# Kernel tuning notes

Hardware: AMD Instinct MI355X
Metric: run time of the kernel (lower is better)

Reference implementation:

```python
import jax, jax.numpy as jnp
import numpy as np

N_EMBD = 2048
HEAD_SIZE = 64  # ln1.weight.shape[0] // n_head = 2048 // 32


def setup_inputs() -> dict:
    key = jax.random.key(0)
    ks = jax.random.split(key, 10)
    B, S, D = 4, 2048, N_EMBD
    return {
        'x': jax.random.normal(ks[0], (B, S, D), jnp.float32),
        'state': jax.random.normal(ks[1], (B, 2 + HEAD_SIZE, D), jnp.float32),
        'time_maa_x': jax.random.uniform(ks[2], (D,), jnp.float32),
        'time_maa_w1': jax.random.normal(ks[3], (D, 160), jnp.float32) * 0.02,
        'time_maa_w2': jax.random.normal(ks[4], (5, 32, D), jnp.float32) * 0.02,
        'maa_k': jax.random.uniform(ks[5], (D,), jnp.float32),
        'maa_w': jax.random.uniform(ks[6], (D,), jnp.float32),
        'maa_v': jax.random.uniform(ks[7], (D,), jnp.float32),
        'maa_r': jax.random.uniform(ks[8], (D,), jnp.float32),
        'maa_g': jax.random.uniform(ks[9], (D,), jnp.float32),
        'i': 0,
    }


def reference(x, state, time_maa_x, time_maa_w1, time_maa_w2,
              maa_k, maa_w, maa_v, maa_r, maa_g, i):
    B, S, D = x.shape
    i1 = (2 + HEAD_SIZE) * i + 1  # state row holding last token of this layer
    # token shift: sx[t] = x[t-1] - x[t], with state row for t=0
    sx = jnp.concatenate([(state[:, i1] - x[:, 0])[:, None],
                          x[:, :-1] - x[:, 1:]], axis=1)  # [B,S,D]
    new_state = state.at[:, i1].set(x[:, -1])
    # LoRA-style mixing coefficients
    xxx = jnp.tanh((x + sx * time_maa_x) @ time_maa_w1)       # [B,S,160]
    xxx = xxx.reshape(B, S, 5, 32)
    xxx = jnp.einsum('bsfk,fkd->bsfd', xxx, time_maa_w2)      # [B,S,5,D]
    stacked = jnp.stack([maa_k, maa_w, maa_v, maa_r, maa_g], axis=0)  # [5,D]
    # broadcast combine across the 5 mixing modes (k,w,v,r,g)
    x_kwvrg = x[:, :, None] + sx[:, :, None] * (stacked + xxx)  # [B,S,5,D]
    return x_kwvrg, new_state
```

## Files before the change

kernel.cpp:

```cpp
#include <hip/hip_runtime.h>

#define DDIM 2048
#define SLEN 2048
#define BSZ 4
#define NTOK (BSZ*SLEN)
#define RANK 160
#define SROWS 66
#define OUT_MAIN ((size_t)NTOK*5*DDIM)
#define STATE_N (BSZ*SROWS*DDIM)

typedef __bf16 bf16x8 __attribute__((ext_vector_type(8)));
typedef float  f32x4  __attribute__((ext_vector_type(4)));
typedef unsigned short us8 __attribute__((ext_vector_type(8)));
typedef unsigned short us4 __attribute__((ext_vector_type(4)));

__device__ __forceinline__ unsigned short f2bf(float f) {
    unsigned b = __float_as_uint(f);
    return (unsigned short)((b + 0x7fffu + ((b >> 16) & 1u)) >> 16);
}

__global__ __launch_bounds__(256) void k_prep(
        const float* __restrict__ x,
        const float* __restrict__ state,
        const int* __restrict__ pi,
        const float* __restrict__ w1,
        const float* __restrict__ w2,
        float* __restrict__ out_state,
        unsigned short* __restrict__ w1t,
        unsigned short* __restrict__ w2t) {
    __shared__ float t[32 * 33];
    int bid = blockIdx.x, tid = threadIdx.x;
    if (bid < 320) {
        int kt = bid / 5;
        int k0 = kt * 32, n0 = (bid - kt * 5) * 32;
        int rr = tid >> 3, cc = (tid & 7) * 4;
        f32x4 v = *(const f32x4*)(w1 + (size_t)(k0 + rr) * RANK + n0 + cc);
        #pragma unroll
        for (int j = 0; j < 4; j++) t[(cc + j) * 33 + rr] = v[j];
        __syncthreads();
        us4 o;
        #pragma unroll
        for (int j = 0; j < 4; j++) o[j] = f2bf(t[rr * 33 + cc + j]);
        *(us4*)(w1t + (size_t)(n0 + rr) * DDIM + k0 + cc) = o;
    } else if (bid < 640) {
        int b2 = bid - 320;
        int f = b2 >> 6, d0 = (b2 & 63) * 32;
        int rr = tid >> 3, cc = (tid & 7) * 4;
        f32x4 v = *(const f32x4*)(w2 + (size_t)(f * 32 + rr) * DDIM + d0 + cc);
        #pragma unroll
        for (int j = 0; j < 4; j++) t[(cc + j) * 33 + rr] = v[j];
        __syncthreads();
        us4 o;
        #pragma unroll
        for (int j = 0; j < 4; j++) o[j] = f2bf(t[rr * 33 + cc + j]);
        *(us4*)(w2t + ((size_t)(f * DDIM) + d0 + rr) * 32 + cc) = o;
    } else {
        int idx = ((bid - 640) * 256 + tid) * 4;
        int i1 = 66 * pi[0] + 1;
        int b   = idx / (SROWS * DDIM);
        int rem = idx - b * (SROWS * DDIM);
        int row = rem / DDIM;
        int d   = rem - row * DDIM;
        f32x4 v;
        if (row == i1) v = *(const f32x4*)(x + ((size_t)(b * SLEN + SLEN - 1)) * DDIM + d);
        else           v = *(const f32x4*)(state + idx);
        *(f32x4*)(out_state + idx) = v;
    }
}

__global__ __launch_bounds__(640) void k_gemm1f(
        const float* __restrict__ x,
        const float* __restrict__ state,
        const float* __restrict__ tmx,
        const unsigned short* __restrict__ w1t,
        const int* __restrict__ pi,
        unsigned short* __restrict__ xxx) {
    __shared__ unsigned short sxw[16 * 136];
    __shared__ float red[10 * 16 * 17];
    int tid  = threadIdx.x;
    int w    = tid >> 6, lane = tid & 63;
    int q    = lane >> 4, nl = lane & 15;
    int kh   = (w >= 5) ? 1 : 0;
    int nh   = kh ? (w - 5) : w;
    int m0   = blockIdx.x * 16;
    int b    = m0 >> 11;
    int i1   = 66 * pi[0] + 1;

    int srow = tid >> 5;
    int scol = (tid & 31) * 4;
    const float* xrow = nullptr;
    const float* prow = nullptr;
    if (tid < 512) {
        int m = m0 + srow;
        int s = m & (SLEN - 1);
        xrow = x + (size_t)m * DDIM;
        prow = (s == 0) ? (state + (size_t)(b * SROWS + i1) * DDIM)
                        : (x + (size_t)(m - 1) * DDIM);
    }

    f32x4 acc[2];
    acc[0] = (f32x4){0.f, 0.f, 0.f, 0.f};
    acc[1] = (f32x4){0.f, 0.f, 0.f, 0.f};

    for (int i = 0; i < 16; i++) {
        if (tid < 512) {
            int gc = i * 128 + scol;
            f32x4 xa = *(const f32x4*)(xrow + gc);
            f32x4 pa = *(const f32x4*)(prow + gc);
            f32x4 ta = *(const f32x4*)(tmx  + gc);
            us4 o;
            #pragma unroll
            for (int j = 0; j < 4; j++)
                o[j] = f2bf(xa[j] + (pa[j] - xa[j]) * ta[j]);
            *(us4*)(sxw + srow * 136 + scol) = o;
        }
        __syncthreads();
        #pragma unroll
        for (int kk = 0; kk < 64; kk += 32) {
            bf16x8 a = *(const bf16x8*)(sxw + nl * 136 + kh * 64 + kk + q * 8);
            #pragma unroll
            for (int t = 0; t < 2; t++) {
                bf16x8 bb = *(const bf16x8*)(w1t + (size_t)(nh * 32 + t * 16 + nl) * DDIM
                                             + i * 128 + kh * 64 + kk + q * 8);
                acc[t] = __builtin_amdgcn_mfma_f32_16x16x32_bf16(a, bb, acc[t], 0, 0, 0);
            }
        }
        __syncthreads();
    }

    if (kh) {
        #pragma unroll
        for (int t = 0; t < 2; t++)
            #pragma unroll
            for (int r = 0; r < 4; r++)
                red[((nh * 2 + t) * 16 + q * 4 + r) * 17 + nl] = acc[t][r];
    }
    __syncthreads();
    if (!kh) {
        #pragma unroll
        for (int t = 0; t < 2; t++)
            #pragma unroll
            for (int r = 0; r < 4; r++) {
                float v = acc[t][r] + red[((nh * 2 + t) * 16 + q * 4 + r) * 17 + nl];
                xxx[(size_t)(m0 + q * 4 + r) * RANK + nh * 32 + t * 16 + nl]
                    = f2bf(tanhf(v));
            }
    }
}

__global__ __launch_bounds__(256) void k_gemm2_out(
        const unsigned short* __restrict__ xxx,
        const unsigned short* __restrict__ w2t,
        const float* __restrict__ x,
        const float* __restrict__ state,
        const float* __restrict__ mk,
        const float* __restrict__ mw,
        const float* __restrict__ mv,
        const float* __restrict__ mr,
        const float* __restrict__ mg,
        const int* __restrict__ pi,
        float* __restrict__ out) {
    __shared__ float res[5 * 16 * 132];
    int tid = threadIdx.x;
    int w = tid >> 6, lane = tid & 63;
    int q = lane >> 4, nl = lane & 15;
    int tokTile = blockIdx.x >> 4;
    int dTile   = blockIdx.x & 15;
    int m0 = tokTile * 16;
    int d0 = dTile * 128;

    for (int t = w; t < 40; t += 4) {
        int f = t >> 3, dsub = t & 7;
        bf16x8 a = *(const bf16x8*)(xxx + (size_t)(m0 + nl) * RANK + f * 32 + q * 8);
        bf16x8 b = *(const bf16x8*)(w2t + ((size_t)(f * DDIM) + d0 + dsub * 16 + nl) * 32 + q * 8);
        f32x4 acc = (f32x4){0.f, 0.f, 0.f, 0.f};
        acc = __builtin_amdgcn_mfma_f32_16x16x32_bf16(a, b, acc, 0, 0, 0);
        #pragma unroll
        for (int r = 0; r < 4; r++)
            res[(f * 16 + q * 4 + r) * 132 + dsub * 16 + nl] = acc[r];
    }
    __syncthreads();

    int i1 = 66 * pi[0] + 1;
    int b     = m0 >> 11;
    int sbase = m0 & (SLEN - 1);
    #pragma unroll
    for (int half = 0; half < 2; half++) {
        int tt  = half * 256 + tid;
        int tok = tt >> 5;
        int dv  = (tt & 31) * 4;
        int s   = sbase + tok;
        int d   = d0 + dv;
        size_t xoff = ((size_t)(b * SLEN + s)) * DDIM + d;
        f32x4 xv = *(const f32x4*)(x + xoff);
        f32x4 pv;
        if (s == 0) pv = *(const f32x4*)(state + ((size_t)(b * SROWS + i1)) * DDIM + d);
        else        pv = *(const f32x4*)(x + xoff - DDIM);
        size_t obase = ((size_t)((b * SLEN + s) * 5)) * DDIM + d;
        #pragma unroll
        for (int f = 0; f < 5; f++) {
            const float* maa = (f == 0) ? mk : (f == 1) ? mw : (f == 2) ? mv
                             : (f == 3) ? mr : mg;
            f32x4 mvv = *(const f32x4*)(maa + d);
            f32x4 rr  = *(const f32x4*)&res[(f * 16 + tok) * 132 + dv];
            f32x4 o;
            #pragma unroll
            for (int j = 0; j < 4; j++) {
                float xf = xv[j];
                float sx = pv[j] - xf;
                o[j] = xf + sx * (mvv[j] + rr[j]);
            }
            *(f32x4*)(out + obase + (size_t)f * DDIM) = o;
        }
    }
}

extern "C" void kernel_launch(void* const* d_in, const int* in_sizes, int n_in,
                              void* d_out, int out_size, void* d_ws, size_t ws_size,
                              hipStream_t stream) {
    const float* x   = (const float*)d_in[0];
    const float* st  = (const float*)d_in[1];
    const float* tmx = (const float*)d_in[2];
    const float* w1  = (const float*)d_in[3];
    const float* w2  = (const float*)d_in[4];
    const float* mk  = (const float*)d_in[5];
    const float* mw  = (const float*)d_in[6];
    const float* mv  = (const float*)d_in[7];
    const float* mr  = (const float*)d_in[8];
    const float* mg  = (const float*)d_in[9];
    const int* pi    = (const int*)d_in[10];
    float* out = (float*)d_out;

    char* ws = (char*)d_ws;
    unsigned short* xxx = (unsigned short*)(ws);
    unsigned short* w1t = (unsigned short*)(ws + 2621440);
    unsigned short* w2t = (unsigned short*)(ws + 2621440 + 655360);

    k_prep<<<1168, 256, 0, stream>>>(x, st, pi, w1, w2, out + OUT_MAIN, w1t, w2t);
    k_gemm1f<<<512, 640, 0, stream>>>(x, st, tmx, w1t, pi, xxx);
    k_gemm2_out<<<8192, 256, 0, stream>>>(xxx, w2t, x, st, mk, mw, mv, mr, mg, pi, out);
}
```

Measured before the change: 459.6 us.

## Fuse LoRA GEMM1, tanh, GEMM2 and output mixing into one kernel

Merges the first projection GEMM (with tanh) and the second per-mode GEMM plus mixing epilogue into a single kernel per 16-token tile. The bf16 intermediate stays in shared memory instead of making a global round trip, and one launch is removed. Each of 5 waves handles one mixing mode and streams across all 2048 channels with scalar nontemporal stores. This gives far fewer blocks and narrower memory accesses than the previous 8192-block epilogue, which risks underusing bandwidth.

```diff
diff --git a/kernel.cpp b/kernel.cpp
--- a/kernel.cpp
+++ b/kernel.cpp
@@ -68,91 +68,12 @@
     }
 }
 
-__global__ __launch_bounds__(640) void k_gemm1f(
+__global__ __launch_bounds__(320, 4) void k_fused(
         const float* __restrict__ x,
         const float* __restrict__ state,
         const float* __restrict__ tmx,
         const unsigned short* __restrict__ w1t,
-        const int* __restrict__ pi,
-        unsigned short* __restrict__ xxx) {
-    __shared__ unsigned short sxw[16 * 136];
-    __shared__ float red[10 * 16 * 17];
-    int tid  = threadIdx.x;
-    int w    = tid >> 6, lane = tid & 63;
-    int q    = lane >> 4, nl = lane & 15;
-    int kh   = (w >= 5) ? 1 : 0;
-    int nh   = kh ? (w - 5) : w;
-    int m0   = blockIdx.x * 16;
-    int b    = m0 >> 11;
-    int i1   = 66 * pi[0] + 1;
-
-    int srow = tid >> 5;
-    int scol = (tid & 31) * 4;
-    const float* xrow = nullptr;
-    const float* prow = nullptr;
-    if (tid < 512) {
-        int m = m0 + srow;
-        int s = m & (SLEN - 1);
-        xrow = x + (size_t)m * DDIM;
-        prow = (s == 0) ? (state + (size_t)(b * SROWS + i1) * DDIM)
-                        : (x + (size_t)(m - 1) * DDIM);
-    }
-
-    f32x4 acc[2];
-    acc[0] = (f32x4){0.f, 0.f, 0.f, 0.f};
-    acc[1] = (f32x4){0.f, 0.f, 0.f, 0.f};
-
-    for (int i = 0; i < 16; i++) {
-        if (tid < 512) {
-            int gc = i * 128 + scol;
-            f32x4 xa = *(const f32x4*)(xrow + gc);
-            f32x4 pa = *(const f32x4*)(prow + gc);
-            f32x4 ta = *(const f32x4*)(tmx  + gc);
-            us4 o;
-            #pragma unroll
-            for (int j = 0; j < 4; j++)
-                o[j] = f2bf(xa[j] + (pa[j] - xa[j]) * ta[j]);
-            *(us4*)(sxw + srow * 136 + scol) = o;
-        }
-        __syncthreads();
-        #pragma unroll
-        for (int kk = 0; kk < 64; kk += 32) {
-            bf16x8 a = *(const bf16x8*)(sxw + nl * 136 + kh * 64 + kk + q * 8);
-            #pragma unroll
-            for (int t = 0; t < 2; t++) {
-                bf16x8 bb = *(const bf16x8*)(w1t + (size_t)(nh * 32 + t * 16 + nl) * DDIM
-                                             + i * 128 + kh * 64 + kk + q * 8);
-                acc[t] = __builtin_amdgcn_mfma_f32_16x16x32_bf16(a, bb, acc[t], 0, 0, 0);
-            }
-        }
-        __syncthreads();
-    }
-
-    if (kh) {
-        #pragma unroll
-        for (int t = 0; t < 2; t++)
-            #pragma unroll
-            for (int r = 0; r < 4; r++)
-                red[((nh * 2 + t) * 16 + q * 4 + r) * 17 + nl] = acc[t][r];
-    }
-    __syncthreads();
-    if (!kh) {
-        #pragma unroll
-        for (int t = 0; t < 2; t++)
-            #pragma unroll
-            for (int r = 0; r < 4; r++) {
-                float v = acc[t][r] + red[((nh * 2 + t) * 16 + q * 4 + r) * 17 + nl];
-                xxx[(size_t)(m0 + q * 4 + r) * RANK + nh * 32 + t * 16 + nl]
-                    = f2bf(tanhf(v));
-            }
-    }
-}
-
-__global__ __launch_bounds__(256) void k_gemm2_out(
-        const unsigned short* __restrict__ xxx,
         const unsigned short* __restrict__ w2t,
-        const float* __restrict__ x,
-        const float* __restrict__ state,
         const float* __restrict__ mk,
         const float* __restrict__ mw,
         const float* __restrict__ mv,
@@ -160,57 +81,121 @@
         const float* __restrict__ mg,
         const int* __restrict__ pi,
         float* __restrict__ out) {
-    __shared__ float res[5 * 16 * 132];
-    int tid = threadIdx.x;
-    int w = tid >> 6, lane = tid & 63;
-    int q = lane >> 4, nl = lane & 15;
-    int tokTile = blockIdx.x >> 4;
-    int dTile   = blockIdx.x & 15;
-    int m0 = tokTile * 16;
-    int d0 = dTile * 128;
-
-    for (int t = w; t < 40; t += 4) {
-        int f = t >> 3, dsub = t & 7;
-        bf16x8 a = *(const bf16x8*)(xxx + (size_t)(m0 + nl) * RANK + f * 32 + q * 8);
-        bf16x8 b = *(const bf16x8*)(w2t + ((size_t)(f * DDIM) + d0 + dsub * 16 + nl) * 32 + q * 8);
-        f32x4 acc = (f32x4){0.f, 0.f, 0.f, 0.f};
-        acc = __builtin_amdgcn_mfma_f32_16x16x32_bf16(a, b, acc, 0, 0, 0);
-        #pragma unroll
-        for (int r = 0; r < 4; r++)
-            res[(f * 16 + q * 4 + r) * 132 + dsub * 16 + nl] = acc[r];
-    }
-    __syncthreads();
-
-    int i1 = 66 * pi[0] + 1;
-    int b     = m0 >> 11;
-    int sbase = m0 & (SLEN - 1);
-    #pragma unroll
-    for (int half = 0; half < 2; half++) {
-        int tt  = half * 256 + tid;
-        int tok = tt >> 5;
-        int dv  = (tt & 31) * 4;
-        int s   = sbase + tok;
-        int d   = d0 + dv;
-        size_t xoff = ((size_t)(b * SLEN + s)) * DDIM + d;
-        f32x4 xv = *(const f32x4*)(x + xoff);
-        f32x4 pv;
-        if (s == 0) pv = *(const f32x4*)(state + ((size_t)(b * SROWS + i1)) * DDIM + d);
-        else        pv = *(const f32x4*)(x + xoff - DDIM);
-        size_t obase = ((size_t)((b * SLEN + s) * 5)) * DDIM + d;
-        #pragma unroll
-        for (int f = 0; f < 5; f++) {
-            const float* maa = (f == 0) ? mk : (f == 1) ? mw : (f == 2) ? mv
-                             : (f == 3) ? mr : mg;
-            f32x4 mvv = *(const f32x4*)(maa + d);
-            f32x4 rr  = *(const f32x4*)&res[(f * 16 + tok) * 132 + dv];
-            f32x4 o;
+    __shared__ unsigned short sxw[16 * 136];
+    __shared__ unsigned short xxxt[16 * 168];
+
+    int tid  = threadIdx.x;
+    int w    = tid >> 6, lane = tid & 63;
+    int q    = lane >> 4, nl = lane & 15;
+    int m0   = blockIdx.x * 16;
+    int b    = m0 >> 11;
+    int i1   = 66 * pi[0] + 1;
+
+    int srow = tid >> 4;
+    int scol = (tid & 15) * 8;
+    const float* xrow = nullptr;
+    const float* prow = nullptr;
+    if (tid < 256) {
+        int m = m0 + srow;
+        int s = m & (SLEN - 1);
+        xrow = x + (size_t)m * DDIM;
+        prow = (s == 0) ? (state + (size_t)(b * SROWS + i1) * DDIM)
+                        : (x + (size_t)(m - 1) * DDIM);
+    }
+
+    f32x4 acc0 = (f32x4){0.f, 0.f, 0.f, 0.f};
+    f32x4 acc1 = (f32x4){0.f, 0.f, 0.f, 0.f};
+
+    for (int k0 = 0; k0 < DDIM; k0 += 128) {
+        if (tid < 256) {
+            f32x4 xa = *(const f32x4*)(xrow + k0 + scol);
+            f32x4 xb = *(const f32x4*)(xrow + k0 + scol + 4);
+            f32x4 pa = *(const f32x4*)(prow + k0 + scol);
+            f32x4 pb = *(const f32x4*)(prow + k0 + scol + 4);
+            f32x4 ta = *(const f32x4*)(tmx  + k0 + scol);
+            f32x4 tb = *(const f32x4*)(tmx  + k0 + scol + 4);
+            us8 o;
             #pragma unroll
             for (int j = 0; j < 4; j++) {
-                float xf = xv[j];
-                float sx = pv[j] - xf;
-                o[j] = xf + sx * (mvv[j] + rr[j]);
-            }
-            *(f32x4*)(out + obase + (size_t)f * DDIM) = o;
+                o[j]     = f2bf(xa[j] + (pa[j] - xa[j]) * ta[j]);
+                o[j + 4] = f2bf(xb[j] + (pb[j] - xb[j]) * tb[j]);
+            }
+            *(us8*)(sxw + srow * 136 + scol) = o;
+        }
+        __syncthreads();
+        #pragma unroll
+        for (int kk = 0; kk < 128; kk += 32) {
+            bf16x8 a  = *(const bf16x8*)(sxw + nl * 136 + kk + q * 8);
+            bf16x8 b0 = *(const bf16x8*)(w1t + (size_t)(w * 32 + nl) * DDIM + k0 + kk + q * 8);
+            bf16x8 b1 = *(const bf16x8*)(w1t + (size_t)(w * 32 + 16 + nl) * DDIM + k0 + kk + q * 8);
+            acc0 = __builtin_amdgcn_mfma_f32_16x16x32_bf16(a, b0, acc0, 0, 0, 0);
+            acc1 = __builtin_amdgcn_mfma_f32_16x16x32_bf16(a, b1, acc1, 0, 0, 0);
+        }
+        __syncthreads();
+    }
+
+    #pragma unroll
+    for (int r = 0; r < 4; r++) {
+        xxxt[(q * 4 + r) * 168 + w * 32 + nl]      = f2bf(tanhf(acc0[r]));
+        xxxt[(q * 4 + r) * 168 + w * 32 + 16 + nl] = f2bf(tanhf(acc1[r]));
+    }
+    __syncthreads();
+
+    const float* maa = (w == 0) ? mk : (w == 1) ? mw : (w == 2) ? mv
+                     : (w == 3) ? mr : mg;
+    bf16x8 af = *(const bf16x8*)(xxxt + nl * 168 + w * 32 + q * 8);
+
+    const float* xb0; const float* xb1; const float* xb2; const float* xb3;
+    const float* pb0; const float* pb1; const float* pb2; const float* pb3;
+    float* ob0; float* ob1; float* ob2; float* ob3;
+    {
+        const float* strow = state + (size_t)(b * SROWS + i1) * DDIM;
+        int t0 = q * 4;
+        int m_ = m0 + t0;
+        xb0 = x + (size_t)m_ * DDIM;
+        pb0 = ((m_ & (SLEN - 1)) == 0) ? strow : (x + (size_t)(m_ - 1) * DDIM);
+        ob0 = (float*)out + ((size_t)(m_ * 5 + w)) * DDIM;
+        m_ = m0 + t0 + 1;
+        xb1 = x + (size_t)m_ * DDIM;
+        pb1 = x + (size_t)(m_ - 1) * DDIM;
+        ob1 = (float*)out + ((size_t)(m_ * 5 + w)) * DDIM;
+        m_ = m0 + t0 + 2;
+        xb2 = x + (size_t)m_ * DDIM;
+        pb2 = x + (size_t)(m_ - 1) * DDIM;
+        ob2 = (float*)out + ((size_t)(m_ * 5 + w)) * DDIM;
+        m_ = m0 + t0 + 3;
+        xb3 = x + (size_t)m_ * DDIM;
+        pb3 = x + (size_t)(m_ - 1) * DDIM;
+        ob3 = (float*)out + ((size_t)(m_ * 5 + w)) * DDIM;
+    }
+
+    const unsigned short* w2base = w2t + ((size_t)w * DDIM) * 32;
+
+    for (int dT = 0; dT < 16; dT++) {
+        int d0 = dT * 128;
+        #pragma unroll 2
+        for (int dsub = 0; dsub < 8; dsub++) {
+            int d = d0 + dsub * 16 + nl;
+            bf16x8 bb = *(const bf16x8*)(w2base + (size_t)d * 32 + q * 8);
+            f32x4 c = (f32x4){0.f, 0.f, 0.f, 0.f};
+            c = __builtin_amdgcn_mfma_f32_16x16x32_bf16(af, bb, c, 0, 0, 0);
+            float ma = maa[d];
+            {
+                float xf = xb0[d], pf = pb0[d];
+                __builtin_nontemporal_store(xf + (pf - xf) * (ma + c[0]), ob0 + d);
+            }
+            {
+                float xf = xb1[d], pf = pb1[d];
+                __builtin_nontemporal_store(xf + (pf - xf) * (ma + c[1]), ob1 + d);
+            }
+            {
+                float xf = xb2[d], pf = pb2[d];
+                __builtin_nontemporal_store(xf + (pf - xf) * (ma + c[2]), ob2 + d);
+            }
+            {
+                float xf = xb3[d], pf = pb3[d];
+                __builtin_nontemporal_store(xf + (pf - xf) * (ma + c[3]), ob3 + d);
+            }
         }
     }
 }
@@ -232,11 +217,10 @@
     float* out = (float*)d_out;
 
     char* ws = (char*)d_ws;
-    unsigned short* xxx = (unsigned short*)(ws);
-    unsigned short* w1t = (unsigned short*)(ws + 2621440);
-    unsigned short* w2t = (unsigned short*)(ws + 2621440 + 655360);
+    unsigned short* w1t = (unsigned short*)(ws);
+    unsigned short* w2t = (unsigned short*)(ws + 655360);
 
     k_prep<<<1168, 256, 0, stream>>>(x, st, pi, w1, w2, out + OUT_MAIN, w1t, w2t);
-    k_gemm1f<<<512, 640, 0, stream>>>(x, st, tmx, w1t, pi, xxx);
-    k_gemm2_out<<<8192, 256, 0, stream>>>(xxx, w2t, x, st, mk, mw, mv, mr, mg, pi, out);
-}
+    k_fused<<<512, 320, 0, stream>>>(x, st, tmx, w1t, w2t,
+                                     mk, mw, mv, mr, mg, pi, out);
+}
```

Measured after the change: 483.5 us. 1.05x slower.
